# Performance work log

Hardware: AMD Instinct MI355X
Metric: run time of the kernel (lower is better)

Reference implementation:

```python
import jax, jax.numpy as jnp
import numpy as np

D, DFFN, H, P, L = 256, 1024, 8, 4, 4
B, LQ = 32, 300
LENS = [2048, 1024, 512, 256]
STARTS = [0, 2048, 3072, 3584]
S = sum(LENS)


def setup_inputs() -> dict:
    key = jax.random.key(0)
    ks = iter(jax.random.split(key, 64))
    def W(shape, s=0.02):
        return jax.random.normal(next(ks), shape, jnp.float32) * s
    inp = {}
    inp['tgt'] = W((B, LQ, D), 1.0)
    inp['query_pos'] = W((B, LQ, D), 1.0)
    centers = jax.random.uniform(next(ks), (B, LQ, L))
    widths = 0.05 + 0.2 * jax.random.uniform(next(ks), (B, LQ, L))
    inp['reference_points'] = jnp.stack([centers, widths], -1)  # (B,Lq,L,2) = (center,width)
    inp['src'] = W((B, S, D), 1.0)
    inp['temporal_lengths'] = np.array(LENS, np.int64)
    inp['level_start_index'] = np.array(STARTS, np.int64)
    for n, shape in [('sa_qw', (D, D)), ('sa_kw', (D, D)), ('sa_vw', (D, D)), ('sa_ow', (D, D)), ('ff1_w', (D, DFFN)), ('ff2_w', (DFFN, D))]:
        inp[n] = W(shape)
    for n, sz in [('sa_qb', D), ('sa_kb', D), ('sa_vb', D), ('sa_ob', D), ('ff1_b', DFFN), ('ff2_b', D)]:
        inp[n] = jnp.zeros((sz,), jnp.float32)
    for pre in ['ca', 'se']:
        inp[pre + '_off_w'] = W((D, H * L * P))
        inp[pre + '_off_b'] = jnp.zeros((H * L * P,), jnp.float32)
        inp[pre + '_attn_w'] = W((D, H * L * P))
        inp[pre + '_attn_b'] = jnp.zeros((H * L * P,), jnp.float32)
        inp[pre + '_val_w'] = W((D, D))
        inp[pre + '_val_b'] = jnp.zeros((D,), jnp.float32)
        inp[pre + '_out_w'] = W((D, D))
        inp[pre + '_out_b'] = jnp.zeros((D,), jnp.float32)
    for n in ['ln1', 'lnse', 'ln2', 'ln3']:
        inp[n + '_g'] = jnp.ones((D,), jnp.float32)
        inp[n + '_b'] = jnp.zeros((D,), jnp.float32)
    return inp


def _ln(x, g, b, eps=1e-5):
    m = jnp.mean(x, -1, keepdims=True)
    v = jnp.mean((x - m) ** 2, -1, keepdims=True)
    return (x - m) * jax.lax.rsqrt(v + eps) * g + b


def _mha(q, k, v, qw, qb, kw, kb, vw, vb, ow, ob):
    b, lq, d = q.shape
    dh = d // H
    qh = (q @ qw + qb).reshape(b, lq, H, dh).transpose(0, 2, 1, 3)
    kh = (k @ kw + kb).reshape(b, -1, H, dh).transpose(0, 2, 1, 3)
    vh = (v @ vw + vb).reshape(b, -1, H, dh).transpose(0, 2, 1, 3)
    scores = jnp.einsum('bhqd,bhkd->bhqk', qh, kh) * (dh ** -0.5)
    attn = jax.nn.softmax(scores, -1)
    out = jnp.einsum('bhqk,bhkd->bhqd', attn, vh).transpose(0, 2, 1, 3).reshape(b, lq, d)
    return out @ ow + ob


def _deform(q, ref, src, lens, starts, vw, vb, offw, offb, aw, ab, ow, ob, boundary):
    b, lq, d = q.shape
    dh = d // H
    value = (src @ vw + vb).reshape(b, -1, H, dh)  # (B,S,H,Dh)
    off = (q @ offw + offb).reshape(b, lq, H, L, P)
    attn = jax.nn.softmax((q @ aw + ab).reshape(b, lq, H, L * P), -1).reshape(b, lq, H, L, P)
    center = ref[..., 0][:, :, None, :, None]  # (B,Lq,1,L,1)
    width = ref[..., 1][:, :, None, :, None]
    if boundary:
        # half the points anchored at segment start, half at segment end
        sign = jnp.where(jnp.arange(P) < P // 2, -0.5, 0.5)
        anchor = center + sign * width
    else:
        anchor = center
    loc = anchor + off / P * width * 0.5  # normalized sampling locations (B,Lq,H,L,P)
    out = jnp.zeros((b, lq, H, dh), value.dtype)
    for l in range(L):
        T = int(lens[l]); s0 = int(starts[l])
        v = value[:, s0:s0 + T].transpose(0, 2, 1, 3)  # (B,H,T,Dh)
        x = loc[:, :, :, l, :] * T - 0.5  # align_corners=False grid
        x0 = jnp.floor(x)
        w = x - x0
        i0 = x0.astype(jnp.int32)
        i1 = i0 + 1
        m0 = ((i0 >= 0) & (i0 < T)).astype(v.dtype)
        m1 = ((i1 >= 0) & (i1 < T)).astype(v.dtype)
        i0c = jnp.clip(i0, 0, T - 1)
        i1c = jnp.clip(i1, 0, T - 1)
        def gather(idx):
            idxh = idx.transpose(0, 2, 1, 3).reshape(b, H, lq * P, 1)
            g = jnp.take_along_axis(v, jnp.broadcast_to(idxh, (b, H, lq * P, dh)), axis=2)
            return g.reshape(b, H, lq, P, dh).transpose(0, 2, 1, 3, 4)  # (B,Lq,H,P,Dh)
        samp = gather(i0c) * ((1 - w) * m0)[..., None] + gather(i1c) * (w * m1)[..., None]
        out = out + jnp.einsum('bqhp,bqhpd->bqhd', attn[:, :, :, l, :], samp)
    return out.reshape(b, lq, d) @ ow + ob


def reference(tgt, query_pos, reference_points, src, temporal_lengths, level_start_index,
              sa_qw, sa_qb, sa_kw, sa_kb, sa_vw, sa_vb, sa_ow, sa_ob,
              ca_off_w, ca_off_b, ca_attn_w, ca_attn_b, ca_val_w, ca_val_b, ca_out_w, ca_out_b,
              se_off_w, se_off_b, se_attn_w, se_attn_b, se_val_w, se_val_b, se_out_w, se_out_b,
              ff1_w, ff1_b, ff2_w, ff2_b,
              ln1_g, ln1_b, lnse_g, lnse_b, ln2_g, ln2_b, ln3_g, ln3_b):
    lens = np.asarray(temporal_lengths)
    starts = np.asarray(level_start_index)
    q = tgt + query_pos
    t2 = _mha(q, q, tgt, sa_qw, sa_qb, sa_kw, sa_kb, sa_vw, sa_vb, sa_ow, sa_ob)
    tgt = _ln(tgt + t2, ln2_g, ln2_b)
    t2 = _deform(tgt + query_pos, reference_points, src, lens, starts,
                 ca_val_w, ca_val_b, ca_off_w, ca_off_b, ca_attn_w, ca_attn_b, ca_out_w, ca_out_b, False)
    tgt = _ln(tgt + t2, ln1_g, ln1_b)
    t2 = _deform(tgt + query_pos, reference_points, src, lens, starts,
                 se_val_w, se_val_b, se_off_w, se_off_b, se_attn_w, se_attn_b, se_out_w, se_out_b, True)
    tgt = _ln(tgt + t2, lnse_g, lnse_b)
    t2 = jax.nn.relu(tgt @ ff1_w + ff1_b) @ ff2_w + ff2_b
    tgt = _ln(tgt + t2, ln3_g, ln3_b)
    return tgt
```

## Files before the change

kernel.cpp:

```cpp
#include <hip/hip_runtime.h>
#include <hip/hip_bf16.h>

namespace {

typedef unsigned short u16;
typedef unsigned int u32;

constexpr int D    = 256;
constexpr int H    = 8;
constexpr int DH   = 32;
constexpr int L    = 4;
constexpr int P    = 4;
constexpr int B    = 32;
constexpr int LQ   = 300;
constexpr int NQ   = B * LQ;
constexpr int S    = 3840;
constexpr int MS   = B * S;
constexpr int DFFN = 1024;

typedef __attribute__((ext_vector_type(8))) short bf16x8;
typedef __attribute__((ext_vector_type(4))) float f32x4;

__device__ inline u16 f2b(float x) {
  u32 u = __builtin_bit_cast(u32, x);
  u32 r = (u + 0x7FFFu + ((u >> 16) & 1u)) >> 16;
  return (u16)r;
}
__device__ inline u32 pk2(float a, float b) {
  return (u32)f2b(a) | ((u32)f2b(b) << 16);
}
__device__ inline void unpack2(u32 w, float& a, float& b) {
  a = __builtin_bit_cast(float, w << 16);
  b = __builtin_bit_cast(float, w & 0xffff0000u);
}

template<bool OUT_BF16, bool RELU>
__global__ __launch_bounds__(256) void gemm_sm(
    const u16* __restrict__ A, const u16* __restrict__ Bt,
    const float* __restrict__ bias, void* __restrict__ Cv,
    int M, int K, int N)
{
  constexpr int BM = 64, BN = 64, BK = 64, LDK = 72;
  __shared__ __align__(16) u16 sh[(BM + BN) * LDK];
  u16* As = sh;
  u16* Bs = sh + BM * LDK;
  const int tid  = threadIdx.x;
  const int lane = tid & 63;
  const int wid  = tid >> 6;
  const int wm = wid >> 1, wn = wid & 1;
  const int m0 = blockIdx.y * BM, n0 = blockIdx.x * BN;

  f32x4 acc[2][2] = {};
  uint4 ra[2], rb[2];
  const int NT = K / BK;
  const int srow = tid >> 3, sch = (tid & 7) * 8;

#pragma unroll
  for (int i = 0; i < 2; ++i) {
    const int row = srow + i * 32;
    ra[i] = *(const uint4*)(A  + (size_t)(m0 + row) * K + sch);
    rb[i] = *(const uint4*)(Bt + (size_t)(n0 + row) * K + sch);
  }

  for (int t = 0; t < NT; ++t) {
#pragma unroll
    for (int i = 0; i < 2; ++i) {
      const int row = srow + i * 32;
      *(uint4*)(&As[row * LDK + sch]) = ra[i];
      *(uint4*)(&Bs[row * LDK + sch]) = rb[i];
    }
    __syncthreads();
    if (t + 1 < NT) {
      const int k0 = (t + 1) * BK;
#pragma unroll
      for (int i = 0; i < 2; ++i) {
        const int row = srow + i * 32;
        ra[i] = *(const uint4*)(A  + (size_t)(m0 + row) * K + k0 + sch);
        rb[i] = *(const uint4*)(Bt + (size_t)(n0 + row) * K + k0 + sch);
      }
    }
#pragma unroll
    for (int kk = 0; kk < 2; ++kk) {
      const int krd = kk * 32 + (lane >> 4) * 8;
      bf16x8 af[2], bf[2];
#pragma unroll
      for (int m = 0; m < 2; ++m)
        af[m] = *(const bf16x8*)(&As[(wm * 32 + (lane & 15) + 16 * m) * LDK + krd]);
#pragma unroll
      for (int n = 0; n < 2; ++n)
        bf[n] = *(const bf16x8*)(&Bs[(wn * 32 + (lane & 15) + 16 * n) * LDK + krd]);
#pragma unroll
      for (int m = 0; m < 2; ++m)
#pragma unroll
        for (int n = 0; n < 2; ++n)
          acc[m][n] = __builtin_amdgcn_mfma_f32_16x16x32_bf16(af[m], bf[n], acc[m][n], 0, 0, 0);
    }
    __syncthreads();
  }

  const int cr = (lane >> 4) * 4;
  const int cc = lane & 15;
  if constexpr (OUT_BF16) {
    u16* stg = sh;
#pragma unroll
    for (int n = 0; n < 2; ++n) {
      const int lc = wn * 32 + n * 16 + cc;
      const float bv = bias[n0 + lc];
#pragma unroll
      for (int m = 0; m < 2; ++m) {
        const int lr0 = wm * 32 + m * 16 + cr;
#pragma unroll
        for (int r = 0; r < 4; ++r) {
          float x = acc[m][n][r] + bv;
          if (RELU) x = fmaxf(x, 0.f);
          stg[(lr0 + r) * LDK + lc] = f2b(x);
        }
      }
    }
    __syncthreads();
    u16* Cb = (u16*)Cv;
#pragma unroll
    for (int i = 0; i < 2; ++i) {
      const int c = tid + 256 * i;
      const int row = c >> 3, ch = c & 7;
      *(uint4*)(Cb + (size_t)(m0 + row) * N + n0 + ch * 8) =
          *(const uint4*)(&stg[row * LDK + ch * 8]);
    }
  } else {
#pragma unroll
    for (int n = 0; n < 2; ++n) {
      const int gc = n0 + wn * 32 + n * 16 + cc;
      const float bv = bias[gc];
#pragma unroll
      for (int m = 0; m < 2; ++m) {
        const int gr0 = m0 + wm * 32 + m * 16 + cr;
#pragma unroll
        for (int r = 0; r < 4; ++r) {
          float x = acc[m][n][r] + bv;
          if (RELU) x = fmaxf(x, 0.f);
          ((float*)Cv)[(size_t)(gr0 + r) * N + gc] = x;
        }
      }
    }
  }
}

__global__ __launch_bounds__(512) void gemm_val3(
    const float* __restrict__ A, const u16* __restrict__ Bt2,
    const float* __restrict__ bias2, u16* __restrict__ Vca, u16* __restrict__ Vse)
{
  __shared__ __align__(16) char shraw[66560];
  char* Asw = shraw;
  const int tid  = threadIdx.x;
  const int lane = tid & 63;
  const int w    = tid >> 6;
  const int m0   = blockIdx.x * 64;

#pragma unroll
  for (int i = 0; i < 4; ++i) {
    const int idx = tid + 512 * i;
    const int row = idx >> 5, ch = idx & 31;
    const float* ap = A + (size_t)(m0 + row) * 256 + ch * 8;
    const float4 f0 = *(const float4*)(ap);
    const float4 f1 = *(const float4*)(ap + 4);
    uint4 pk;
    pk.x = pk2(f0.x, f0.y); pk.y = pk2(f0.z, f0.w);
    pk.z = pk2(f1.x, f1.y); pk.w = pk2(f1.z, f1.w);
    *(uint4*)(Asw + row * 512 + ((ch * 16) ^ ((row & 7) << 4))) = pk;
  }
  __syncthreads();

  f32x4 acc[4][4] = {};
  const u16* bb = Bt2 + (size_t)(w * 64 + (lane & 15)) * 256 + (lane >> 4) * 8;

#pragma unroll 2
  for (int kk = 0; kk < 8; ++kk) {
    bf16x8 af[4], bf[4];
    const int kb = kk * 64 + (lane >> 4) * 16;
#pragma unroll
    for (int m = 0; m < 4; ++m) {
      const int row = m * 16 + (lane & 15);
      af[m] = *(const bf16x8*)(Asw + row * 512 + (kb ^ ((row & 7) << 4)));
    }
#pragma unroll
    for (int n = 0; n < 4; ++n)
      bf[n] = *(const bf16x8*)(bb + n * 4096 + kk * 32);
#pragma unroll
    for (int m = 0; m < 4; ++m)
#pragma unroll
      for (int n = 0; n < 4; ++n)
        acc[m][n] = __builtin_amdgcn_mfma_f32_16x16x32_bf16(af[m], bf[n], acc[m][n], 0, 0, 0);
  }
  __syncthreads();

  constexpr int STC = 520;
  u16* stg = (u16*)shraw;
  const int cr = (lane >> 4) * 4;
  const int cc = lane & 15;
#pragma unroll
  for (int n = 0; n < 4; ++n) {
    const int col = w * 64 + n * 16 + cc;
    const float bv = bias2[col];
#pragma unroll
    for (int m = 0; m < 4; ++m) {
      const int r0 = m * 16 + cr;
#pragma unroll
      for (int r = 0; r < 4; ++r)
        stg[(r0 + r) * STC + col] = f2b(acc[m][n][r] + bv);
    }
  }
  __syncthreads();
#pragma unroll
  for (int i = 0; i < 8; ++i) {
    const int c = tid + 512 * i;
    const int row = c >> 6, ch = c & 63;
    u16* dst = (ch < 32) ? (Vca + (size_t)(m0 + row) * 256 + ch * 8)
                         : (Vse + (size_t)(m0 + row) * 256 + (ch - 32) * 8);
    *(uint4*)dst = *(const uint4*)(&stg[row * STC + ch * 8]);
  }
}

template<int MODE>
__global__ __launch_bounds__(512) void gemm_ln(
    const u16* __restrict__ A, const u16* __restrict__ Bt,
    const float* __restrict__ bias, const float* __restrict__ res,
    const float* __restrict__ g, const float* __restrict__ be,
    const float* __restrict__ qpos,
    float* __restrict__ fout, u16* __restrict__ bfout, int K)
{
  constexpr int BM = 64, BK = 64, LDK = 72;
  __shared__ __align__(16) float ftile[64 * 264];
  u16* As = (u16*)ftile;
  u16* Bs = As + BM * LDK;
  const int tid  = threadIdx.x;
  const int lane = tid & 63;
  const int wid  = tid >> 6;
  const int wm = wid >> 2, wn = wid & 3;
  const int m0 = blockIdx.x * BM;

  f32x4 acc[2][4] = {};
  const int NT = K / BK;
  const int arow = tid >> 3, ach = (tid & 7) * 8;

  uint4 ra, rb[4];
  ra = *(const uint4*)(A + (size_t)(m0 + arow) * K + ach);
#pragma unroll
  for (int i = 0; i < 4; ++i)
    rb[i] = *(const uint4*)(Bt + (size_t)(arow + 64 * i) * K + ach);

  for (int t = 0; t < NT; ++t) {
    *(uint4*)(&As[arow * LDK + ach]) = ra;
#pragma unroll
    for (int i = 0; i < 4; ++i)
      *(uint4*)(&Bs[(arow + 64 * i) * LDK + ach]) = rb[i];
    __syncthreads();
    if (t + 1 < NT) {
      const int k0 = (t + 1) * BK;
      ra = *(const uint4*)(A + (size_t)(m0 + arow) * K + k0 + ach);
#pragma unroll
      for (int i = 0; i < 4; ++i)
        rb[i] = *(const uint4*)(Bt + (size_t)(arow + 64 * i) * K + k0 + ach);
    }
#pragma unroll
    for (int kk = 0; kk < 2; ++kk) {
      const int krd = kk * 32 + (lane >> 4) * 8;
      bf16x8 af[2], bf[4];
#pragma unroll
      for (int m = 0; m < 2; ++m)
        af[m] = *(const bf16x8*)(&As[(wm * 32 + m * 16 + (lane & 15)) * LDK + krd]);
#pragma unroll
      for (int n = 0; n < 4; ++n)
        bf[n] = *(const bf16x8*)(&Bs[(wn * 64 + n * 16 + (lane & 15)) * LDK + krd]);
#pragma unroll
      for (int m = 0; m < 2; ++m)
#pragma unroll
        for (int n = 0; n < 4; ++n)
          acc[m][n] = __builtin_amdgcn_mfma_f32_16x16x32_bf16(af[m], bf[n], acc[m][n], 0, 0, 0);
    }
    __syncthreads();
  }

  const int cr = (lane >> 4) * 4;
  const int cc = lane & 15;
#pragma unroll
  for (int n = 0; n < 4; ++n) {
    const int col = wn * 64 + n * 16 + cc;
    const float bv = bias[col];
#pragma unroll
    for (int m = 0; m < 2; ++m) {
      const int r0 = wm * 32 + m * 16 + cr;
#pragma unroll
      for (int r = 0; r < 4; ++r)
        ftile[(r0 + r) * 264 + col] = acc[m][n][r] + bv;
    }
  }
  __syncthreads();

  const int row = tid >> 3, s8 = tid & 7;
  const size_t grow = (size_t)(m0 + row) * 256;
  float vv[32];
  float sum = 0.f;
#pragma unroll
  for (int j = 0; j < 8; ++j) {
    const int col = s8 * 4 + j * 32;
    const float4 fv = *(const float4*)(&ftile[row * 264 + col]);
    const float4 rv = *(const float4*)(res + grow + col);
    vv[j * 4 + 0] = fv.x + rv.x; vv[j * 4 + 1] = fv.y + rv.y;
    vv[j * 4 + 2] = fv.z + rv.z; vv[j * 4 + 3] = fv.w + rv.w;
    sum += vv[j * 4 + 0] + vv[j * 4 + 1] + vv[j * 4 + 2] + vv[j * 4 + 3];
  }
  sum += __shfl_xor(sum, 1, 64);
  sum += __shfl_xor(sum, 2, 64);
  sum += __shfl_xor(sum, 4, 64);
  const float mean = sum * (1.f / 256.f);
  float sq = 0.f;
#pragma unroll
  for (int k = 0; k < 32; ++k) { const float d = vv[k] - mean; sq += d * d; }
  sq += __shfl_xor(sq, 1, 64);
  sq += __shfl_xor(sq, 2, 64);
  sq += __shfl_xor(sq, 4, 64);
  const float rstd = rsqrtf(sq * (1.f / 256.f) + 1e-5f);

#pragma unroll
  for (int j = 0; j < 8; ++j) {
    const int col = s8 * 4 + j * 32;
    const float4 gv = *(const float4*)(g + col);
    const float4 bv = *(const float4*)(be + col);
    float4 y;
    y.x = (vv[j * 4 + 0] - mean) * rstd * gv.x + bv.x;
    y.y = (vv[j * 4 + 1] - mean) * rstd * gv.y + bv.y;
    y.z = (vv[j * 4 + 2] - mean) * rstd * gv.z + bv.z;
    y.w = (vv[j * 4 + 3] - mean) * rstd * gv.w + bv.w;
    *(float4*)(fout + grow + col) = y;
    if constexpr (MODE == 0) {
      const float4 qv = *(const float4*)(qpos + grow + col);
      uint2 pk;
      pk.x = pk2(y.x + qv.x, y.y + qv.y);
      pk.y = pk2(y.z + qv.z, y.w + qv.w);
      *(uint2*)(bfout + grow + col) = pk;
    } else if constexpr (MODE == 1) {
      uint2 pk;
      pk.x = pk2(y.x, y.y);
      pk.y = pk2(y.z, y.w);
      *(uint2*)(bfout + grow + col) = pk;
    }
  }
}

struct WSpec { const float* w; u16* wt; int K, N, blk0; };
struct WPack { WSpec s[14]; };

__global__ __launch_bounds__(256) void wt_transpose(WPack p) {
  __shared__ float tile[32][33];
  const int b = blockIdx.x;
  int i = 0;
#pragma unroll
  for (int j = 1; j < 14; ++j) if (b >= p.s[j].blk0) i = j;
  const float* w = p.s[i].w;
  u16* wt = p.s[i].wt;
  const int K = p.s[i].K, N = p.s[i].N;
  const int lb = b - p.s[i].blk0;
  const int ntN = N >> 5;
  const int tk = lb / ntN, tn = lb - tk * ntN;
  const int r = threadIdx.x >> 5, c = threadIdx.x & 31;
#pragma unroll
  for (int j = 0; j < 4; ++j)
    tile[r + j * 8][c] = w[(size_t)(tk * 32 + r + j * 8) * N + tn * 32 + c];
  __syncthreads();
#pragma unroll
  for (int j = 0; j < 4; ++j)
    wt[(size_t)(tn * 32 + r + j * 8) * K + tk * 32 + c] = f2b(tile[c][r + j * 8]);
}

__global__ __launch_bounds__(256) void prep_tgt(
    const float* __restrict__ tgt, const float* __restrict__ qpos,
    u16* __restrict__ tgtb, u16* __restrict__ qbuf, int n4)
{
  int i = blockIdx.x * 256 + threadIdx.x;
  const int stride = gridDim.x * 256;
  for (; i < n4; i += stride) {
    const float4 t = ((const float4*)tgt)[i];
    const float4 q = ((const float4*)qpos)[i];
    uint2 a, b;
    a.x = pk2(t.x, t.y); a.y = pk2(t.z, t.w);
    b.x = pk2(t.x + q.x, t.y + q.y); b.y = pk2(t.z + q.z, t.w + q.w);
    ((uint2*)tgtb)[i] = a;
    ((uint2*)qbuf)[i] = b;
  }
}

__global__ __launch_bounds__(512) void concat_b3(
    const float* ca_off_b, const float* ca_attn_b,
    const float* se_off_b, const float* se_attn_b,
    const float* sa_qb, const float* sa_kb,
    const float* ca_val_b, const float* se_val_b,
    float* __restrict__ bias4, float* __restrict__ qkb, float* __restrict__ valb)
{
  const int t = threadIdx.x;
  bias4[t] = t < 128 ? ca_off_b[t] : t < 256 ? ca_attn_b[t - 128]
           : t < 384 ? se_off_b[t - 256] : se_attn_b[t - 384];
  qkb[t]  = t < 256 ? sa_qb[t] : sa_kb[t - 256];
  valb[t] = t < 256 ? ca_val_b[t] : se_val_b[t - 256];
}

__global__ __launch_bounds__(512) void mha_v2(
    const u16* __restrict__ qk, const u16* __restrict__ vh,
    u16* __restrict__ out)
{
  __shared__ __align__(16) float Ks[8 * 300 * 4];
  __shared__ __align__(16) float Vs[8 * 300 * 4];
  const int bh  = blockIdx.x & 255;
  const int seg = blockIdx.x >> 8;
  const int b = bh >> 3, h = bh & 7;
  const u16* kbase = qk + (size_t)b * LQ * 512 + 256 + h * DH;
  const u16* vbase = vh + (size_t)b * LQ * D + h * DH;
  for (int e = threadIdx.x; e < 300 * 8; e += 512) {
    const int r = e >> 3, j = e & 7;
    float4 f;
    const uint2 kv = *(const uint2*)(kbase + (size_t)r * 512 + j * 4);
    unpack2(kv.x, f.x, f.y);
    unpack2(kv.y, f.z, f.w);
    *(float4*)(&Ks[(j * 300 + r) * 4]) = f;
    const uint2 vv = *(const uint2*)(vbase + (size_t)r * D + j * 4);
    unpack2(vv.x, f.x, f.y);
    unpack2(vv.y, f.z, f.w);
    *(float4*)(&Vs[(j * 300 + r) * 4]) = f;
  }
  __syncthreads();

  const int lane = threadIdx.x & 63;
  const int lq = (threadIdx.x >> 6) * 16 + (lane >> 2);
  const int kc = lane & 3;
  const int q = seg * 128 + lq;
  if (q >= LQ) return;

  const u16* qrow = qk + (size_t)(b * LQ + q) * 512 + h * DH;
  float qv[DH];
#pragma unroll
  for (int c4 = 0; c4 < 4; ++c4) {
    const uint4 u = *(const uint4*)(qrow + c4 * 8);
    unpack2(u.x, qv[c4 * 8 + 0], qv[c4 * 8 + 1]);
    unpack2(u.y, qv[c4 * 8 + 2], qv[c4 * 8 + 3]);
    unpack2(u.z, qv[c4 * 8 + 4], qv[c4 * 8 + 5]);
    unpack2(u.w, qv[c4 * 8 + 6], qv[c4 * 8 + 7]);
  }
#pragma unroll
  for (int d = 0; d < DH; ++d) qv[d] *= 0.17677669529663689f;

  float o[DH] = {};
  float ssum = 0.f;
  const float* kp = &Ks[kc * 75 * 4];
  const float* vp = &Vs[kc * 75 * 4];
  for (int i = 0; i < 75; ++i) {
    float s = 0.f;
#pragma unroll
    for (int j = 0; j < 8; ++j) {
      const float4 kf = *(const float4*)(kp + i * 4 + j * 1200);
      s += qv[j * 4 + 0] * kf.x + qv[j * 4 + 1] * kf.y
         + qv[j * 4 + 2] * kf.z + qv[j * 4 + 3] * kf.w;
    }
    const float p = __expf(s);
    ssum += p;
#pragma unroll
    for (int j = 0; j < 8; ++j) {
      const float4 vf = *(const float4*)(vp + i * 4 + j * 1200);
      o[j * 4 + 0] += p * vf.x; o[j * 4 + 1] += p * vf.y;
      o[j * 4 + 2] += p * vf.z; o[j * 4 + 3] += p * vf.w;
    }
  }

  ssum += __shfl_xor(ssum, 1, 64);
  ssum += __shfl_xor(ssum, 2, 64);
#pragma unroll
  for (int d = 0; d < DH; ++d) {
    o[d] += __shfl_xor(o[d], 1, 64);
    o[d] += __shfl_xor(o[d], 2, 64);
  }
  const float inv = 1.f / ssum;

  u16* orow = out + (size_t)(b * LQ + q) * D + h * DH;
#pragma unroll
  for (int c = 0; c < 4; ++c) {
    if (kc == c) {
      uint4 w;
      w.x = pk2(o[c * 8 + 0] * inv, o[c * 8 + 1] * inv);
      w.y = pk2(o[c * 8 + 2] * inv, o[c * 8 + 3] * inv);
      w.z = pk2(o[c * 8 + 4] * inv, o[c * 8 + 5] * inv);
      w.w = pk2(o[c * 8 + 6] * inv, o[c * 8 + 7] * inv);
      *(uint4*)(orow + c * 8) = w;
    }
  }
}

template<bool BOUNDARY>
__global__ __launch_bounds__(128) void deform_v2(
    const float* __restrict__ oa, const float* __restrict__ ref,
    const u16* __restrict__ value, u16* __restrict__ out)
{
  __shared__ __align__(16) uint4 owt[128];
  const int bq = blockIdx.x;
  const int b = bq / LQ;
  const int t = threadIdx.x;
  const int h = t >> 4;
  const int l = (t >> 2) & 3;
  const int p = t & 3;

  const float off   = oa[(size_t)bq * 256 + t];
  const float logit = oa[(size_t)bq * 256 + 128 + t];
  const float center = ref[(size_t)bq * 8 + l * 2 + 0];
  const float width  = ref[(size_t)bq * 8 + l * 2 + 1];

  const float e = __expf(logit);
  float ssum = e;
  ssum += __shfl_xor(ssum, 1, 64);
  ssum += __shfl_xor(ssum, 2, 64);
  ssum += __shfl_xor(ssum, 4, 64);
  ssum += __shfl_xor(ssum, 8, 64);
  const float wa = e / ssum;

  const int T  = 2048 >> l;
  const int s0 = 4096 - (4096 >> l);
  float anchor = center;
  if (BOUNDARY) anchor += (p < 2 ? -0.5f : 0.5f) * width;
  const float loc = anchor + off * width * 0.125f;
  const float x = loc * (float)T - 0.5f;
  const float x0 = floorf(x);
  const float w = x - x0;
  const int i0 = (int)x0;
  const int i1 = i0 + 1;
  const float w0 = (i0 >= 0 && i0 < T) ? wa * (1.f - w) : 0.f;
  const float w1 = (i1 >= 0 && i1 < T) ? wa * w : 0.f;
  const int i0c = min(max(i0, 0), T - 1);
  const int i1c = min(max(i1, 0), T - 1);
  uint4 pack;
  pack.x = (u32)((s0 + i0c) * (D * 2) + h * (DH * 2));
  pack.y = __builtin_bit_cast(u32, w0);
  pack.z = (u32)((s0 + i1c) * (D * 2) + h * (DH * 2));
  pack.w = __builtin_bit_cast(u32, w1);
  owt[t] = pack;
  __syncthreads();

  const int g  = t >> 4;
  const int ln = t & 15;
  const char* vb = (const char*)(value + (size_t)b * S * D) + ln * 4;
  float o0 = 0.f, o1 = 0.f;
#pragma unroll
  for (int j = 0; j < 16; ++j) {
    const uint4 ow = owt[g * 16 + j];
    const u32 v0 = *(const u32*)(vb + ow.x);
    const u32 v1 = *(const u32*)(vb + ow.z);
    const float wt0 = __builtin_bit_cast(float, ow.y);
    const float wt1 = __builtin_bit_cast(float, ow.w);
    float a, c;
    unpack2(v0, a, c); o0 += wt0 * a; o1 += wt0 * c;
    unpack2(v1, a, c); o0 += wt1 * a; o1 += wt1 * c;
  }
  const u32 res = pk2(o0, o1);
  *(u32*)(out + (size_t)bq * D + g * DH + ln * 2) = res;
}

}

extern "C" void kernel_launch(void* const* d_in, const int* in_sizes, int n_in,
                              void* d_out, int out_size, void* d_ws, size_t ws_size,
                              hipStream_t stream)
{
  const float* tgt   = (const float*)d_in[0];
  const float* qpos  = (const float*)d_in[1];
  const float* ref   = (const float*)d_in[2];
  const float* src   = (const float*)d_in[3];
  const float* sa_qw = (const float*)d_in[6];
  const float* sa_kw = (const float*)d_in[7];
  const float* sa_vw = (const float*)d_in[8];
  const float* sa_ow = (const float*)d_in[9];
  const float* ff1_w = (const float*)d_in[10];
  const float* ff2_w = (const float*)d_in[11];
  const float* sa_qb = (const float*)d_in[12];
  const float* sa_kb = (const float*)d_in[13];
  const float* sa_vb = (const float*)d_in[14];
  const float* sa_ob = (const float*)d_in[15];
  const float* ff1_b = (const float*)d_in[16];
  const float* ff2_b = (const float*)d_in[17];
  const float* ca_off_w  = (const float*)d_in[18];
  const float* ca_off_b  = (const float*)d_in[19];
  const float* ca_attn_w = (const float*)d_in[20];
  const float* ca_attn_b = (const float*)d_in[21];
  const float* ca_val_w  = (const float*)d_in[22];
  const float* ca_val_b  = (const float*)d_in[23];
  const float* ca_out_w  = (const float*)d_in[24];
  const float* ca_out_b  = (const float*)d_in[25];
  const float* se_off_w  = (const float*)d_in[26];
  const float* se_off_b  = (const float*)d_in[27];
  const float* se_attn_w = (const float*)d_in[28];
  const float* se_attn_b = (const float*)d_in[29];
  const float* se_val_w  = (const float*)d_in[30];
  const float* se_val_b  = (const float*)d_in[31];
  const float* se_out_w  = (const float*)d_in[32];
  const float* se_out_b  = (const float*)d_in[33];
  const float* ln1_g  = (const float*)d_in[34];
  const float* ln1_b  = (const float*)d_in[35];
  const float* lnse_g = (const float*)d_in[36];
  const float* lnse_b = (const float*)d_in[37];
  const float* ln2_g  = (const float*)d_in[38];
  const float* ln2_b  = (const float*)d_in[39];
  const float* ln3_g  = (const float*)d_in[40];
  const float* ln3_b  = (const float*)d_in[41];

  const size_t ND = (size_t)NQ * D;
  const size_t MD = (size_t)MS * D;

  char* base = (char*)d_ws;
  size_t off = 0;
  auto alloc = [&](size_t bytes) -> void* {
    void* p = base + off;
    off += (bytes + 255) & ~(size_t)255;
    return p;
  };
  u16*  Vca  = (u16*)alloc(MD * 2);
  u16*  Vse  = (u16*)alloc(MD * 2);
  u16*  qkbuf = (u16*)alloc((size_t)NQ * 512 * 2);
  u16*  vh   = (u16*)alloc(ND * 2);
  u16*  qbuf = (u16*)alloc(ND * 2);
  u16*  smpb = (u16*)alloc(ND * 2);
  u16*  tgtb = (u16*)alloc(ND * 2);
  u16*  curb = (u16*)alloc(ND * 2);
  float* cur = (float*)alloc(ND * 4);
  float* oabuf = (float*)alloc((size_t)NQ * 256 * 4);
  float* bias4 = (float*)alloc(512 * 4);
  float* qkb   = (float*)alloc(512 * 4);
  float* valb  = (float*)alloc(512 * 4);

  u16* ffh = Vca;

  WPack pk;
  int wi = 0, blk = 0;
  auto addw = [&](const float* w, int K, int N) -> u16* {
    u16* wt = (u16*)alloc((size_t)K * N * 2);
    pk.s[wi].w = w; pk.s[wi].wt = wt; pk.s[wi].K = K; pk.s[wi].N = N; pk.s[wi].blk0 = blk;
    blk += (K / 32) * (N / 32);
    ++wi;
    return wt;
  };
  u16* saq_t = addw(sa_qw, D, D);
  u16* sak_t = addw(sa_kw, D, D);        (void)sak_t;
  u16* sav_t = addw(sa_vw, D, D);
  u16* sao_t = addw(sa_ow, D, D);
  u16* ff1_t = addw(ff1_w, D, DFFN);
  u16* ff2_t = addw(ff2_w, DFFN, D);
  u16* caoff_t = addw(ca_off_w, D, 128);
  u16* caatt_t = addw(ca_attn_w, D, 128);  (void)caatt_t;
  u16* seoff_t = addw(se_off_w, D, 128);
  u16* seatt_t = addw(se_attn_w, D, 128);  (void)seatt_t;
  u16* caval_t = addw(ca_val_w, D, D);
  u16* seval_t = addw(se_val_w, D, D);     (void)seval_t;
  u16* caout_t = addw(ca_out_w, D, D);
  u16* seout_t = addw(se_out_w, D, D);

  const int n4 = (int)(ND / 4);

  concat_b3<<<1, 512, 0, stream>>>(ca_off_b, ca_attn_b, se_off_b, se_attn_b,
                                   sa_qb, sa_kb, ca_val_b, se_val_b,
                                   bias4, qkb, valb);
  wt_transpose<<<blk, 256, 0, stream>>>(pk);
  gemm_val3<<<MS / 64, 512, 0, stream>>>(src, caval_t, valb, Vca, Vse);
  prep_tgt<<<1200, 256, 0, stream>>>(tgt, qpos, tgtb, qbuf, n4);

  gemm_sm<true,  false><<<dim3(8, 150), 256, 0, stream>>>(qbuf, saq_t, qkb, qkbuf, NQ, D, 512);
  gemm_sm<true,  false><<<dim3(4, 150), 256, 0, stream>>>(tgtb, sav_t, sa_vb, vh, NQ, D, D);
  mha_v2<<<B * H * 3, 512, 0, stream>>>(qkbuf, vh, smpb);
  gemm_ln<0><<<NQ / 64, 512, 0, stream>>>(smpb, sao_t, sa_ob, tgt, ln2_g, ln2_b, qpos, cur, qbuf, D);

  gemm_sm<false, false><<<dim3(4, 150), 256, 0, stream>>>(qbuf, caoff_t, bias4, oabuf, NQ, D, 256);
  deform_v2<false><<<NQ, 128, 0, stream>>>(oabuf, ref, Vca, smpb);
  gemm_ln<0><<<NQ / 64, 512, 0, stream>>>(smpb, caout_t, ca_out_b, cur, ln1_g, ln1_b, qpos, cur, qbuf, D);

  gemm_sm<false, false><<<dim3(4, 150), 256, 0, stream>>>(qbuf, seoff_t, bias4 + 256, oabuf, NQ, D, 256);
  deform_v2<true><<<NQ, 128, 0, stream>>>(oabuf, ref, Vse, smpb);
  gemm_ln<1><<<NQ / 64, 512, 0, stream>>>(smpb, seout_t, se_out_b, cur, lnse_g, lnse_b, nullptr, cur, curb, D);

  gemm_sm<true,  true ><<<dim3(16, 150), 256, 0, stream>>>(curb, ff1_t, ff1_b, ffh, NQ, D, DFFN);
  gemm_ln<2><<<NQ / 64, 512, 0, stream>>>(ffh, ff2_t, ff2_b, cur, ln3_g, ln3_b, nullptr, (float*)d_out, nullptr, DFFN);
}
```

Baseline: 478.6 us.

## Merge prep kernels, fuse QKV GEMMs, split value GEMM, widen LN and deform blocks

Folds the bias concat, weight transpose and tgt conversion into one prep launch, and runs the QK and V self-attention projections as a single GEMM launch. The value-projection GEMM is split across two blocks per row tile with prefetched B fragments. gemm_ln grows to 1024 threads, each wave handling 16 rows. deform now packs four queries per 512-thread block. The aim is fewer launches and more parallelism per block, at the cost of more A-tile reloads in the value GEMM and some idle threads in the wider LN kernel.

```diff
diff --git a/kernel.cpp b/kernel.cpp
--- a/kernel.cpp
+++ b/kernel.cpp
@@ -145,16 +145,115 @@
   }
 }
 
-__global__ __launch_bounds__(512) void gemm_val3(
+__global__ __launch_bounds__(256) void gemm_qkv(
+    const u16* __restrict__ qbuf, const u16* __restrict__ tgtb,
+    const u16* __restrict__ saqk_t, const u16* __restrict__ sav_t,
+    const float* __restrict__ qkb, const float* __restrict__ vbias,
+    u16* __restrict__ qkbuf, u16* __restrict__ vh)
+{
+  constexpr int K = 256, BK = 64, LDK = 72;
+  __shared__ __align__(16) u16 sh[128 * LDK];
+  u16* As = sh;
+  u16* Bs = sh + 64 * LDK;
+  const bool isv = blockIdx.x >= 8;
+  const u16* A  = isv ? tgtb : qbuf;
+  const u16* Bt = isv ? sav_t : saqk_t;
+  const float* bias = isv ? vbias : qkb;
+  u16* C = isv ? vh : qkbuf;
+  const int N = isv ? 256 : 512;
+  const int n0 = (isv ? (int)blockIdx.x - 8 : (int)blockIdx.x) * 64;
+  const int m0 = blockIdx.y * 64;
+
+  const int tid  = threadIdx.x;
+  const int lane = tid & 63;
+  const int wid  = tid >> 6;
+  const int wm = wid >> 1, wn = wid & 1;
+
+  f32x4 acc[2][2] = {};
+  uint4 ra[2], rb[2];
+  const int srow = tid >> 3, sch = (tid & 7) * 8;
+
+#pragma unroll
+  for (int i = 0; i < 2; ++i) {
+    const int row = srow + i * 32;
+    ra[i] = *(const uint4*)(A  + (size_t)(m0 + row) * K + sch);
+    rb[i] = *(const uint4*)(Bt + (size_t)(n0 + row) * K + sch);
+  }
+  for (int t = 0; t < 4; ++t) {
+#pragma unroll
+    for (int i = 0; i < 2; ++i) {
+      const int row = srow + i * 32;
+      *(uint4*)(&As[row * LDK + sch]) = ra[i];
+      *(uint4*)(&Bs[row * LDK + sch]) = rb[i];
+    }
+    __syncthreads();
+    if (t + 1 < 4) {
+      const int k0 = (t + 1) * BK;
+#pragma unroll
+      for (int i = 0; i < 2; ++i) {
+        const int row = srow + i * 32;
+        ra[i] = *(const uint4*)(A  + (size_t)(m0 + row) * K + k0 + sch);
+        rb[i] = *(const uint4*)(Bt + (size_t)(n0 + row) * K + k0 + sch);
+      }
+    }
+#pragma unroll
+    for (int kk = 0; kk < 2; ++kk) {
+      const int krd = kk * 32 + (lane >> 4) * 8;
+      bf16x8 af[2], bf[2];
+#pragma unroll
+      for (int m = 0; m < 2; ++m)
+        af[m] = *(const bf16x8*)(&As[(wm * 32 + (lane & 15) + 16 * m) * LDK + krd]);
+#pragma unroll
+      for (int n = 0; n < 2; ++n)
+        bf[n] = *(const bf16x8*)(&Bs[(wn * 32 + (lane & 15) + 16 * n) * LDK + krd]);
+#pragma unroll
+      for (int m = 0; m < 2; ++m)
+#pragma unroll
+        for (int n = 0; n < 2; ++n)
+          acc[m][n] = __builtin_amdgcn_mfma_f32_16x16x32_bf16(af[m], bf[n], acc[m][n], 0, 0, 0);
+    }
+    __syncthreads();
+  }
+
+  const int cr = (lane >> 4) * 4;
+  const int cc = lane & 15;
+  u16* stg = sh;
+#pragma unroll
+  for (int n = 0; n < 2; ++n) {
+    const int lc = wn * 32 + n * 16 + cc;
+    const float bv = bias[n0 + lc];
+#pragma unroll
+    for (int m = 0; m < 2; ++m) {
+      const int lr0 = wm * 32 + m * 16 + cr;
+#pragma unroll
+      for (int r = 0; r < 4; ++r)
+        stg[(lr0 + r) * LDK + lc] = f2b(acc[m][n][r] + bv);
+    }
+  }
+  __syncthreads();
+#pragma unroll
+  for (int i = 0; i < 2; ++i) {
+    const int c = tid + 256 * i;
+    const int row = c >> 3, ch = c & 7;
+    *(uint4*)(C + (size_t)(m0 + row) * N + n0 + ch * 8) =
+        *(const uint4*)(&stg[row * LDK + ch * 8]);
+  }
+}
+
+__global__ __launch_bounds__(512) void gemm_val4(
     const float* __restrict__ A, const u16* __restrict__ Bt2,
     const float* __restrict__ bias2, u16* __restrict__ Vca, u16* __restrict__ Vse)
 {
-  __shared__ __align__(16) char shraw[66560];
+  __shared__ __align__(16) char shraw[33792];
   char* Asw = shraw;
   const int tid  = threadIdx.x;
   const int lane = tid & 63;
   const int w    = tid >> 6;
-  const int m0   = blockIdx.x * 64;
+  const int nh   = blockIdx.x & 1;
+  const int m0   = (blockIdx.x >> 1) * 64;
+  u16* dst = nh ? Vse : Vca;
+  const u16* Bt = Bt2 + nh * 256 * 256;
+  const float* bias = bias2 + nh * 256;
 
 #pragma unroll
   for (int i = 0; i < 4; ++i) {
@@ -170,37 +269,44 @@
   }
   __syncthreads();
 
-  f32x4 acc[4][4] = {};
-  const u16* bb = Bt2 + (size_t)(w * 64 + (lane & 15)) * 256 + (lane >> 4) * 8;
-
-#pragma unroll 2
+  f32x4 acc[4][2] = {};
+  const u16* bb = Bt + (size_t)(w * 32 + (lane & 15)) * 256 + (lane >> 4) * 8;
+  bf16x8 bcur[2], bnxt[2];
+#pragma unroll
+  for (int n = 0; n < 2; ++n) bcur[n] = *(const bf16x8*)(bb + n * 4096);
+
+#pragma unroll
   for (int kk = 0; kk < 8; ++kk) {
-    bf16x8 af[4], bf[4];
+    bf16x8 af[4];
     const int kb = kk * 64 + (lane >> 4) * 16;
 #pragma unroll
     for (int m = 0; m < 4; ++m) {
       const int row = m * 16 + (lane & 15);
       af[m] = *(const bf16x8*)(Asw + row * 512 + (kb ^ ((row & 7) << 4)));
     }
-#pragma unroll
-    for (int n = 0; n < 4; ++n)
-      bf[n] = *(const bf16x8*)(bb + n * 4096 + kk * 32);
+    if (kk < 7) {
+#pragma unroll
+      for (int n = 0; n < 2; ++n)
+        bnxt[n] = *(const bf16x8*)(bb + n * 4096 + (kk + 1) * 32);
+    }
 #pragma unroll
     for (int m = 0; m < 4; ++m)
 #pragma unroll
-      for (int n = 0; n < 4; ++n)
-        acc[m][n] = __builtin_amdgcn_mfma_f32_16x16x32_bf16(af[m], bf[n], acc[m][n], 0, 0, 0);
+      for (int n = 0; n < 2; ++n)
+        acc[m][n] = __builtin_amdgcn_mfma_f32_16x16x32_bf16(af[m], bcur[n], acc[m][n], 0, 0, 0);
+#pragma unroll
+    for (int n = 0; n < 2; ++n) bcur[n] = bnxt[n];
   }
   __syncthreads();
 
-  constexpr int STC = 520;
+  constexpr int STC = 264;
   u16* stg = (u16*)shraw;
   const int cr = (lane >> 4) * 4;
   const int cc = lane & 15;
 #pragma unroll
-  for (int n = 0; n < 4; ++n) {
-    const int col = w * 64 + n * 16 + cc;
-    const float bv = bias2[col];
+  for (int n = 0; n < 2; ++n) {
+    const int col = w * 32 + n * 16 + cc;
+    const float bv = bias[col];
 #pragma unroll
     for (int m = 0; m < 4; ++m) {
       const int r0 = m * 16 + cr;
@@ -211,71 +317,77 @@
   }
   __syncthreads();
 #pragma unroll
-  for (int i = 0; i < 8; ++i) {
+  for (int i = 0; i < 4; ++i) {
     const int c = tid + 512 * i;
-    const int row = c >> 6, ch = c & 63;
-    u16* dst = (ch < 32) ? (Vca + (size_t)(m0 + row) * 256 + ch * 8)
-                         : (Vse + (size_t)(m0 + row) * 256 + (ch - 32) * 8);
-    *(uint4*)dst = *(const uint4*)(&stg[row * STC + ch * 8]);
+    const int row = c >> 5, ch = c & 31;
+    *(uint4*)(dst + (size_t)(m0 + row) * 256 + ch * 8) =
+        *(const uint4*)(&stg[row * STC + ch * 8]);
   }
 }
 
 template<int MODE>
-__global__ __launch_bounds__(512) void gemm_ln(
+__global__ __launch_bounds__(1024) void gemm_ln(
     const u16* __restrict__ A, const u16* __restrict__ Bt,
     const float* __restrict__ bias, const float* __restrict__ res,
     const float* __restrict__ g, const float* __restrict__ be,
     const float* __restrict__ qpos,
     float* __restrict__ fout, u16* __restrict__ bfout, int K)
 {
-  constexpr int BM = 64, BK = 64, LDK = 72;
+  constexpr int BK = 64, LDK = 72;
   __shared__ __align__(16) float ftile[64 * 264];
   u16* As = (u16*)ftile;
-  u16* Bs = As + BM * LDK;
+  u16* Bs = As + 64 * LDK;
   const int tid  = threadIdx.x;
   const int lane = tid & 63;
   const int wid  = tid >> 6;
   const int wm = wid >> 2, wn = wid & 3;
-  const int m0 = blockIdx.x * BM;
-
-  f32x4 acc[2][4] = {};
+  const int m0 = blockIdx.x * 64;
+
+  f32x4 acc[4] = {};
   const int NT = K / BK;
+  const bool am = tid < 512;
   const int arow = tid >> 3, ach = (tid & 7) * 8;
 
-  uint4 ra, rb[4];
-  ra = *(const uint4*)(A + (size_t)(m0 + arow) * K + ach);
-#pragma unroll
-  for (int i = 0; i < 4; ++i)
-    rb[i] = *(const uint4*)(Bt + (size_t)(arow + 64 * i) * K + ach);
+  uint4 ra = {};
+  uint4 rb[2];
+  if (am) ra = *(const uint4*)(A + (size_t)(m0 + arow) * K + ach);
+#pragma unroll
+  for (int i = 0; i < 2; ++i) {
+    const int idx = tid + 1024 * i;
+    const int brow = idx >> 3, bch = (idx & 7) * 8;
+    rb[i] = *(const uint4*)(Bt + (size_t)brow * K + bch);
+  }
 
   for (int t = 0; t < NT; ++t) {
-    *(uint4*)(&As[arow * LDK + ach]) = ra;
-#pragma unroll
-    for (int i = 0; i < 4; ++i)
-      *(uint4*)(&Bs[(arow + 64 * i) * LDK + ach]) = rb[i];
+    if (am) *(uint4*)(&As[arow * LDK + ach]) = ra;
+#pragma unroll
+    for (int i = 0; i < 2; ++i) {
+      const int idx = tid + 1024 * i;
+      const int brow = idx >> 3, bch = (idx & 7) * 8;
+      *(uint4*)(&Bs[brow * LDK + bch]) = rb[i];
+    }
     __syncthreads();
     if (t + 1 < NT) {
       const int k0 = (t + 1) * BK;
-      ra = *(const uint4*)(A + (size_t)(m0 + arow) * K + k0 + ach);
-#pragma unroll
-      for (int i = 0; i < 4; ++i)
-        rb[i] = *(const uint4*)(Bt + (size_t)(arow + 64 * i) * K + k0 + ach);
+      if (am) ra = *(const uint4*)(A + (size_t)(m0 + arow) * K + k0 + ach);
+#pragma unroll
+      for (int i = 0; i < 2; ++i) {
+        const int idx = tid + 1024 * i;
+        const int brow = idx >> 3, bch = (idx & 7) * 8;
+        rb[i] = *(const uint4*)(Bt + (size_t)brow * K + k0 + bch);
+      }
     }
 #pragma unroll
     for (int kk = 0; kk < 2; ++kk) {
       const int krd = kk * 32 + (lane >> 4) * 8;
-      bf16x8 af[2], bf[4];
-#pragma unroll
-      for (int m = 0; m < 2; ++m)
-        af[m] = *(const bf16x8*)(&As[(wm * 32 + m * 16 + (lane & 15)) * LDK + krd]);
+      bf16x8 af, bf[4];
+      af = *(const bf16x8*)(&As[(wm * 16 + (lane & 15)) * LDK + krd]);
 #pragma unroll
       for (int n = 0; n < 4; ++n)
         bf[n] = *(const bf16x8*)(&Bs[(wn * 64 + n * 16 + (lane & 15)) * LDK + krd]);
 #pragma unroll
-      for (int m = 0; m < 2; ++m)
-#pragma unroll
-        for (int n = 0; n < 4; ++n)
-          acc[m][n] = __builtin_amdgcn_mfma_f32_16x16x32_bf16(af[m], bf[n], acc[m][n], 0, 0, 0);
+      for (int n = 0; n < 4; ++n)
+        acc[n] = __builtin_amdgcn_mfma_f32_16x16x32_bf16(af, bf[n], acc[n], 0, 0, 0);
     }
     __syncthreads();
   }
@@ -287,22 +399,18 @@
     const int col = wn * 64 + n * 16 + cc;
     const float bv = bias[col];
 #pragma unroll
-    for (int m = 0; m < 2; ++m) {
-      const int r0 = wm * 32 + m * 16 + cr;
-#pragma unroll
-      for (int r = 0; r < 4; ++r)
-        ftile[(r0 + r) * 264 + col] = acc[m][n][r] + bv;
-    }
+    for (int r = 0; r < 4; ++r)
+      ftile[(wm * 16 + cr + r) * 264 + col] = acc[n][r] + bv;
   }
   __syncthreads();
 
-  const int row = tid >> 3, s8 = tid & 7;
+  const int row = tid >> 4, s16 = tid & 15;
   const size_t grow = (size_t)(m0 + row) * 256;
-  float vv[32];
+  float vv[16];
   float sum = 0.f;
 #pragma unroll
-  for (int j = 0; j < 8; ++j) {
-    const int col = s8 * 4 + j * 32;
+  for (int j = 0; j < 4; ++j) {
+    const int col = s16 * 4 + j * 64;
     const float4 fv = *(const float4*)(&ftile[row * 264 + col]);
     const float4 rv = *(const float4*)(res + grow + col);
     vv[j * 4 + 0] = fv.x + rv.x; vv[j * 4 + 1] = fv.y + rv.y;
@@ -312,18 +420,20 @@
   sum += __shfl_xor(sum, 1, 64);
   sum += __shfl_xor(sum, 2, 64);
   sum += __shfl_xor(sum, 4, 64);
+  sum += __shfl_xor(sum, 8, 64);
   const float mean = sum * (1.f / 256.f);
   float sq = 0.f;
 #pragma unroll
-  for (int k = 0; k < 32; ++k) { const float d = vv[k] - mean; sq += d * d; }
+  for (int k = 0; k < 16; ++k) { const float d = vv[k] - mean; sq += d * d; }
   sq += __shfl_xor(sq, 1, 64);
   sq += __shfl_xor(sq, 2, 64);
   sq += __shfl_xor(sq, 4, 64);
+  sq += __shfl_xor(sq, 8, 64);
   const float rstd = rsqrtf(sq * (1.f / 256.f) + 1e-5f);
 
 #pragma unroll
-  for (int j = 0; j < 8; ++j) {
-    const int col = s8 * 4 + j * 32;
+  for (int j = 0; j < 4; ++j) {
+    const int col = s16 * 4 + j * 64;
     const float4 gv = *(const float4*)(g + col);
     const float4 bv = *(const float4*)(be + col);
     float4 y;
@@ -350,57 +460,57 @@
 struct WSpec { const float* w; u16* wt; int K, N, blk0; };
 struct WPack { WSpec s[14]; };
 
-__global__ __launch_bounds__(256) void wt_transpose(WPack p) {
+struct PrepArgs {
+  const float *ca_off_b, *ca_attn_b, *se_off_b, *se_attn_b;
+  const float *sa_qb, *sa_kb, *ca_val_b, *se_val_b;
+  float *bias4, *qkb, *valb;
+  const float *tgt, *qpos;
+  u16 *tgtb, *qbuf;
+  int n4, nwt;
+};
+
+__global__ __launch_bounds__(256) void prep_all(WPack p, PrepArgs a) {
   __shared__ float tile[32][33];
   const int b = blockIdx.x;
-  int i = 0;
-#pragma unroll
-  for (int j = 1; j < 14; ++j) if (b >= p.s[j].blk0) i = j;
-  const float* w = p.s[i].w;
-  u16* wt = p.s[i].wt;
-  const int K = p.s[i].K, N = p.s[i].N;
-  const int lb = b - p.s[i].blk0;
-  const int ntN = N >> 5;
-  const int tk = lb / ntN, tn = lb - tk * ntN;
-  const int r = threadIdx.x >> 5, c = threadIdx.x & 31;
-#pragma unroll
-  for (int j = 0; j < 4; ++j)
-    tile[r + j * 8][c] = w[(size_t)(tk * 32 + r + j * 8) * N + tn * 32 + c];
-  __syncthreads();
-#pragma unroll
-  for (int j = 0; j < 4; ++j)
-    wt[(size_t)(tn * 32 + r + j * 8) * K + tk * 32 + c] = f2b(tile[c][r + j * 8]);
-}
-
-__global__ __launch_bounds__(256) void prep_tgt(
-    const float* __restrict__ tgt, const float* __restrict__ qpos,
-    u16* __restrict__ tgtb, u16* __restrict__ qbuf, int n4)
-{
-  int i = blockIdx.x * 256 + threadIdx.x;
-  const int stride = gridDim.x * 256;
-  for (; i < n4; i += stride) {
-    const float4 t = ((const float4*)tgt)[i];
-    const float4 q = ((const float4*)qpos)[i];
-    uint2 a, b;
-    a.x = pk2(t.x, t.y); a.y = pk2(t.z, t.w);
-    b.x = pk2(t.x + q.x, t.y + q.y); b.y = pk2(t.z + q.z, t.w + q.w);
-    ((uint2*)tgtb)[i] = a;
-    ((uint2*)qbuf)[i] = b;
-  }
-}
-
-__global__ __launch_bounds__(512) void concat_b3(
-    const float* ca_off_b, const float* ca_attn_b,
-    const float* se_off_b, const float* se_attn_b,
-    const float* sa_qb, const float* sa_kb,
-    const float* ca_val_b, const float* se_val_b,
-    float* __restrict__ bias4, float* __restrict__ qkb, float* __restrict__ valb)
-{
-  const int t = threadIdx.x;
-  bias4[t] = t < 128 ? ca_off_b[t] : t < 256 ? ca_attn_b[t - 128]
-           : t < 384 ? se_off_b[t - 256] : se_attn_b[t - 384];
-  qkb[t]  = t < 256 ? sa_qb[t] : sa_kb[t - 256];
-  valb[t] = t < 256 ? ca_val_b[t] : se_val_b[t - 256];
+  if (b < a.nwt) {
+    int i = 0;
+#pragma unroll
+    for (int j = 1; j < 14; ++j) if (b >= p.s[j].blk0) i = j;
+    const float* w = p.s[i].w;
+    u16* wt = p.s[i].wt;
+    const int K = p.s[i].K, N = p.s[i].N;
+    const int lb = b - p.s[i].blk0;
+    const int ntN = N >> 5;
+    const int tk = lb / ntN, tn = lb - tk * ntN;
+    const int r = threadIdx.x >> 5, c = threadIdx.x & 31;
+#pragma unroll
+    for (int j = 0; j < 4; ++j)
+      tile[r + j * 8][c] = w[(size_t)(tk * 32 + r + j * 8) * N + tn * 32 + c];
+    __syncthreads();
+#pragma unroll
+    for (int j = 0; j < 4; ++j)
+      wt[(size_t)(tn * 32 + r + j * 8) * K + tk * 32 + c] = f2b(tile[c][r + j * 8]);
+  } else if (b == a.nwt) {
+#pragma unroll
+    for (int u = 0; u < 2; ++u) {
+      const int t = threadIdx.x + 256 * u;
+      a.bias4[t] = t < 128 ? a.ca_off_b[t] : t < 256 ? a.ca_attn_b[t - 128]
+                 : t < 384 ? a.se_off_b[t - 256] : a.se_attn_b[t - 384];
+      a.qkb[t]  = t < 256 ? a.sa_qb[t] : a.sa_kb[t - 256];
+      a.valb[t] = t < 256 ? a.ca_val_b[t] : a.se_val_b[t - 256];
+    }
+  } else {
+    const int i = (b - a.nwt - 1) * 256 + threadIdx.x;
+    if (i < a.n4) {
+      const float4 t = ((const float4*)a.tgt)[i];
+      const float4 q = ((const float4*)a.qpos)[i];
+      uint2 x, y;
+      x.x = pk2(t.x, t.y); x.y = pk2(t.z, t.w);
+      y.x = pk2(t.x + q.x, t.y + q.y); y.y = pk2(t.z + q.z, t.w + q.w);
+      ((uint2*)a.tgtb)[i] = x;
+      ((uint2*)a.qbuf)[i] = y;
+    }
+  }
 }
 
 __global__ __launch_bounds__(512) void mha_v2(
@@ -493,14 +603,15 @@
 }
 
 template<bool BOUNDARY>
-__global__ __launch_bounds__(128) void deform_v2(
+__global__ __launch_bounds__(512) void deform_v2(
     const float* __restrict__ oa, const float* __restrict__ ref,
     const u16* __restrict__ value, u16* __restrict__ out)
 {
-  __shared__ __align__(16) uint4 owt[128];
-  const int bq = blockIdx.x;
+  __shared__ __align__(16) uint4 owt[4][128];
+  const int unit = threadIdx.x >> 7;
+  const int bq = blockIdx.x * 4 + unit;
   const int b = bq / LQ;
-  const int t = threadIdx.x;
+  const int t = threadIdx.x & 127;
   const int h = t >> 4;
   const int l = (t >> 2) & 3;
   const int p = t & 3;
@@ -537,7 +648,7 @@
   pack.y = __builtin_bit_cast(u32, w0);
   pack.z = (u32)((s0 + i1c) * (D * 2) + h * (DH * 2));
   pack.w = __builtin_bit_cast(u32, w1);
-  owt[t] = pack;
+  owt[unit][t] = pack;
   __syncthreads();
 
   const int g  = t >> 4;
@@ -546,7 +657,7 @@
   float o0 = 0.f, o1 = 0.f;
 #pragma unroll
   for (int j = 0; j < 16; ++j) {
-    const uint4 ow = owt[g * 16 + j];
+    const uint4 ow = owt[unit][g * 16 + j];
     const u32 v0 = *(const u32*)(vb + ow.x);
     const u32 v1 = *(const u32*)(vb + ow.z);
     const float wt0 = __builtin_bit_cast(float, ow.y);
@@ -658,26 +769,29 @@
 
   const int n4 = (int)(ND / 4);
 
-  concat_b3<<<1, 512, 0, stream>>>(ca_off_b, ca_attn_b, se_off_b, se_attn_b,
-                                   sa_qb, sa_kb, ca_val_b, se_val_b,
-                                   bias4, qkb, valb);
-  wt_transpose<<<blk, 256, 0, stream>>>(pk);
-  gemm_val3<<<MS / 64, 512, 0, stream>>>(src, caval_t, valb, Vca, Vse);
-  prep_tgt<<<1200, 256, 0, stream>>>(tgt, qpos, tgtb, qbuf, n4);
-
-  gemm_sm<true,  false><<<dim3(8, 150), 256, 0, stream>>>(qbuf, saq_t, qkb, qkbuf, NQ, D, 512);
-  gemm_sm<true,  false><<<dim3(4, 150), 256, 0, stream>>>(tgtb, sav_t, sa_vb, vh, NQ, D, D);
+  PrepArgs pa;
+  pa.ca_off_b = ca_off_b; pa.ca_attn_b = ca_attn_b;
+  pa.se_off_b = se_off_b; pa.se_attn_b = se_attn_b;
+  pa.sa_qb = sa_qb; pa.sa_kb = sa_kb; pa.ca_val_b = ca_val_b; pa.se_val_b = se_val_b;
+  pa.bias4 = bias4; pa.qkb = qkb; pa.valb = valb;
+  pa.tgt = tgt; pa.qpos = qpos; pa.tgtb = tgtb; pa.qbuf = qbuf;
+  pa.n4 = n4; pa.nwt = blk;
+  prep_all<<<blk + 1 + 2400, 256, 0, stream>>>(pk, pa);
+
+  gemm_val4<<<(MS / 64) * 2, 512, 0, stream>>>(src, caval_t, valb, Vca, Vse);
+
+  gemm_qkv<<<dim3(12, 150), 256, 0, stream>>>(qbuf, tgtb, saq_t, sav_t, qkb, sa_vb, qkbuf, vh);
   mha_v2<<<B * H * 3, 512, 0, stream>>>(qkbuf, vh, smpb);
-  gemm_ln<0><<<NQ / 64, 512, 0, stream>>>(smpb, sao_t, sa_ob, tgt, ln2_g, ln2_b, qpos, cur, qbuf, D);
+  gemm_ln<0><<<NQ / 64, 1024, 0, stream>>>(smpb, sao_t, sa_ob, tgt, ln2_g, ln2_b, qpos, cur, qbuf, D);
 
   gemm_sm<false, false><<<dim3(4, 150), 256, 0, stream>>>(qbuf, caoff_t, bias4, oabuf, NQ, D, 256);
-  deform_v2<false><<<NQ, 128, 0, stream>>>(oabuf, ref, Vca, smpb);
-  gemm_ln<0><<<NQ / 64, 512, 0, stream>>>(smpb, caout_t, ca_out_b, cur, ln1_g, ln1_b, qpos, cur, qbuf, D);
+  deform_v2<false><<<NQ / 4, 512, 0, stream>>>(oabuf, ref, Vca, smpb);
+  gemm_ln<0><<<NQ / 64, 1024, 0, stream>>>(smpb, caout_t, ca_out_b, cur, ln1_g, ln1_b, qpos, cur, qbuf, D);
 
   gemm_sm<false, false><<<dim3(4, 150), 256, 0, stream>>>(qbuf, seoff_t, bias4 + 256, oabuf, NQ, D, 256);
-  deform_v2<true><<<NQ, 128, 0, stream>>>(oabuf, ref, Vse, smpb);
-  gemm_ln<1><<<NQ / 64, 512, 0, stream>>>(smpb, seout_t, se_out_b, cur, lnse_g, lnse_b, nullptr, cur, curb, D);
+  deform_v2<true><<<NQ / 4, 512, 0, stream>>>(oabuf, ref, Vse, smpb);
+  gemm_ln<1><<<NQ / 64, 1024, 0, stream>>>(smpb, seout_t, se_out_b, cur, lnse_g, lnse_b, nullptr, cur, curb, D);
 
   gemm_sm<true,  true ><<<dim3(16, 150), 256, 0, stream>>>(curb, ff1_t, ff1_b, ffh, NQ, D, DFFN);
-  gemm_ln<2><<<NQ / 64, 512, 0, stream>>>(ffh, ff2_t, ff2_b, cur, ln3_g, ln3_b, nullptr, (float*)d_out, nullptr, DFFN);
-}
+  gemm_ln<2><<<NQ / 64, 1024, 0, stream>>>(ffh, ff2_t, ff2_b, cur, ln3_g, ln3_b, nullptr, (float*)d_out, nullptr, DFFN);
+}
```

Measured after the change: 474.0 us. Within noise of the previous version (-1.0%).
